# Optimization experiments

Measured on AMD Instinct MI355X. Metric: run time of the kernel, lower is better.

The kernel has to match this reference:

```python
import jax, jax.numpy as jnp
import numpy as np

N_NODES = 100000
N_EDGES = 300000
D_IN = 256
D_OUT = 256
NEG_SLOPE = 0.2


def setup_inputs() -> dict:
    key = jax.random.key(0)
    ks = jax.random.split(key, 6)
    feat = jax.random.normal(ks[0], (N_NODES, D_IN), dtype=jnp.float32)
    # xavier-normal-ish init scale
    scale = (2.0 / (D_IN + D_OUT)) ** 0.5
    W_src = jax.random.normal(ks[1], (D_IN, D_OUT), dtype=jnp.float32) * scale
    b_src = jnp.zeros((D_OUT,), dtype=jnp.float32)
    W_dst = jax.random.normal(ks[2], (D_IN, D_OUT), dtype=jnp.float32) * scale
    b_dst = jnp.zeros((D_OUT,), dtype=jnp.float32)
    attn = jax.random.normal(ks[3], (D_OUT,), dtype=jnp.float32) * scale
    src = jax.random.randint(ks[4], (N_EDGES,), 0, N_NODES, dtype=jnp.int32)
    dst = jax.random.randint(ks[5], (N_EDGES,), 0, N_NODES, dtype=jnp.int32)
    return {"feat": feat, "W_src": W_src, "b_src": b_src,
            "W_dst": W_dst, "b_dst": b_dst, "attn": attn,
            "src": src, "dst": dst}


def reference(feat, W_src, b_src, W_dst, b_dst, attn, src, dst):
    N = feat.shape[0]
    # node projections (dense GEMMs)
    el = feat @ W_src + b_src          # [N, D_OUT]  (feat_src / 'el')
    er = feat @ W_dst + b_dst          # [N, D_OUT]  (feat_dst / 'er')
    # edge-wise u_add_v + LeakyReLU, then attention dot
    e = jax.nn.leaky_relu(el[src] + er[dst], NEG_SLOPE)  # [E, D_OUT]
    score = e @ attn                    # [E]  ((e*attn).sum(-1))
    # edge softmax segmented by destination node
    smax = jax.ops.segment_max(score, dst, num_segments=N)   # [N]
    ex = jnp.exp(score - smax[dst])                           # [E]
    ssum = jax.ops.segment_sum(ex, dst, num_segments=N)      # [N]
    a = ex / ssum[dst]                                        # [E]
    # weighted scatter-sum aggregation: u_mul_e('el','a') -> sum per dst
    out = jax.ops.segment_sum(el[src] * a[:, None], dst, num_segments=N)
    return out  # [N, D_OUT]
```

## Files before the change

kernel.cpp:

```cpp
#include <hip/hip_runtime.h>
#include <cstdint>
#include <cmath>

#define D 256
#define NEG 0.2f
#define BK 64
#define NT (D/BK)

typedef __attribute__((ext_vector_type(8))) __bf16 bf16x8;
typedef __attribute__((ext_vector_type(8))) unsigned short ushort8;
typedef __attribute__((ext_vector_type(4))) float f32x4;

__device__ __forceinline__ unsigned short f2bf(float f){
    unsigned u = __float_as_uint(f);
    return (unsigned short)((u + 0x7fffu + ((u >> 16) & 1u)) >> 16);
}
__device__ __forceinline__ float b2f(unsigned short u){
    return __uint_as_float(((unsigned)u) << 16);
}

__device__ __forceinline__ void gload_lds16(const void* g, void* l){
    __builtin_amdgcn_global_load_lds(
        (const __attribute__((address_space(1))) unsigned int*)g,
        (__attribute__((address_space(3))) unsigned int*)l, 16, 0, 0);
}

__global__ __launch_bounds__(256) void prep_w_kernel(
    const float* __restrict__ Wsrc, const float* __restrict__ Wdst,
    const float* __restrict__ bsrc, const float* __restrict__ bdst,
    unsigned short* __restrict__ WT, float* __restrict__ biascat)
{
    int idx = blockIdx.x*256 + threadIdx.x;
    int col = idx >> 5;
    int u   = idx & 31;
    int gu  = (u & 24) | ((u ^ col) & 7);
    const float* W = (col < 256) ? Wsrc : Wdst;
    int c = col & 255;
    ushort8 o;
    #pragma unroll
    for (int j = 0; j < 8; ++j)
        o[j] = f2bf(W[(size_t)(gu*8 + j)*D + c]);
    *(ushort8*)(WT + (size_t)col*D + u*8) = o;
    if (idx < 512) biascat[idx] = (idx < 256) ? bsrc[idx] : bdst[idx-256];
}

__global__ __launch_bounds__(256) void prep_feat_kernel(
    const float* __restrict__ feat, unsigned short* __restrict__ featb, int N, int NPAD)
{
    int total = NPAD * 32;
    for (int idx = blockIdx.x*256 + threadIdx.x; idx < total; idx += gridDim.x*256){
        int r = idx >> 5;
        int u = idx & 31;
        ushort8 o;
        if (r < N){
            int gu = (u & 24) | ((u ^ r) & 7);
            const float* s = feat + (size_t)r*D + gu*8;
            float4 a = *(const float4*)s;
            float4 b = *(const float4*)(s + 4);
            o[0]=f2bf(a.x); o[1]=f2bf(a.y); o[2]=f2bf(a.z); o[3]=f2bf(a.w);
            o[4]=f2bf(b.x); o[5]=f2bf(b.y); o[6]=f2bf(b.z); o[7]=f2bf(b.w);
        } else {
            #pragma unroll
            for (int j = 0; j < 8; ++j) o[j] = 0;
        }
        *(ushort8*)(featb + (size_t)r*D + u*8) = o;
    }
}

__global__ __launch_bounds__(256) void proj_mfma_kernel(
    const unsigned short* __restrict__ featb, const unsigned short* __restrict__ WT,
    const float* __restrict__ biascat,
    unsigned short* __restrict__ el16, unsigned short* __restrict__ er16, int N)
{
    __shared__ unsigned short As[2][128*BK];
    __shared__ unsigned short Bs[2][128*BK];

    const int b    = blockIdx.x;
    const int xcd  = b & 7;
    const int s    = b >> 3;
    const int p    = (s >> 2)*8 + xcd;
    const int c    = s & 3;
    const int row0 = p * 128;
    const int col0 = c * 128;

    const int tid  = threadIdx.x;
    const int wave = tid >> 6;
    const int lane = tid & 63;
    const int wr = (wave >> 1) * 64;
    const int wc = (wave & 1) * 64;
    const int l15 = lane & 15;
    const int kg  = lane >> 4;

    const int sr = (wave << 3) + (lane >> 3);
    const int sc = (lane & 7) * 8;

    f32x4 acc[4][4] = {};

    #pragma unroll
    for (int r4 = 0; r4 < 4; ++r4) {
        int ar = r4*32 + sr;
        gload_lds16(featb + (size_t)(row0 + ar)*D + 0 + sc, &As[0][(r4*32 + wave*8)*BK]);
        gload_lds16(WT    + (size_t)(col0 + ar)*D + 0 + sc, &Bs[0][(r4*32 + wave*8)*BK]);
    }

    for (int t = 0; t < NT; ++t) {
        const int cur = t & 1;
        if (t + 1 < NT) {
            int k0 = (t + 1) * BK;
            #pragma unroll
            for (int r4 = 0; r4 < 4; ++r4) {
                int ar = r4*32 + sr;
                gload_lds16(featb + (size_t)(row0 + ar)*D + k0 + sc,
                            &As[cur ^ 1][(r4*32 + wave*8)*BK]);
                gload_lds16(WT    + (size_t)(col0 + ar)*D + k0 + sc,
                            &Bs[cur ^ 1][(r4*32 + wave*8)*BK]);
            }
            asm volatile("s_waitcnt vmcnt(8)" ::: "memory");
        } else {
            asm volatile("s_waitcnt vmcnt(0)" ::: "memory");
        }
        __builtin_amdgcn_s_barrier();
        __builtin_amdgcn_sched_barrier(0);

        #pragma unroll
        for (int ks = 0; ks < 2; ++ks) {
            bf16x8 af[4], bfr[4];
            #pragma unroll
            for (int m = 0; m < 4; ++m){
                int row = wr + m*16 + l15;
                int cc = ((kg + ks*4) ^ (row & 7)) * 8;
                af[m] = *(const bf16x8*)&As[cur][row*BK + cc];
            }
            #pragma unroll
            for (int n = 0; n < 4; ++n){
                int row = wc + n*16 + l15;
                int cc = ((kg + ks*4) ^ (row & 7)) * 8;
                bfr[n] = *(const bf16x8*)&Bs[cur][row*BK + cc];
            }
            #pragma unroll
            for (int m = 0; m < 4; ++m)
                #pragma unroll
                for (int n = 0; n < 4; ++n)
                    acc[m][n] = __builtin_amdgcn_mfma_f32_16x16x32_bf16(bfr[n], af[m], acc[m][n], 0, 0, 0);
        }
        __builtin_amdgcn_sched_barrier(0);
        __builtin_amdgcn_s_barrier();
    }

    unsigned short* __restrict__ dstp = (col0 < 256) ? el16 : er16;
    const int ccbase = col0 & 255;
    #pragma unroll
    for (int m = 0; m < 4; ++m) {
        int row = row0 + wr + m*16 + l15;
        if (row >= N) continue;
        #pragma unroll
        for (int n = 0; n < 4; ++n) {
            int cw = wc + n*16 + kg*4;
            float4 b4 = *(const float4*)(biascat + col0 + cw);
            ushort4 o;
            o.x = f2bf(acc[m][n][0] + b4.x);
            o.y = f2bf(acc[m][n][1] + b4.y);
            o.z = f2bf(acc[m][n][2] + b4.z);
            o.w = f2bf(acc[m][n][3] + b4.w);
            *(ushort4*)(dstp + (size_t)row*D + ccbase + cw) = o;
        }
    }
}

__global__ void count_kernel(const int* __restrict__ dst, int* __restrict__ deg, int E){
    int e = blockIdx.x*blockDim.x + threadIdx.x;
    if (e < E) atomicAdd(&deg[dst[e]], 1);
}

__global__ __launch_bounds__(256) void scan1_kernel(const int* __restrict__ deg,
                                                    int* __restrict__ incl,
                                                    int* __restrict__ bsum, int N){
    __shared__ int s[256];
    int i = blockIdx.x*256 + threadIdx.x;
    int v = (i < N) ? deg[i] : 0;
    s[threadIdx.x] = v;
    __syncthreads();
    #pragma unroll
    for (int off = 1; off < 256; off <<= 1){
        int t = (threadIdx.x >= off) ? s[threadIdx.x - off] : 0;
        __syncthreads();
        s[threadIdx.x] += t;
        __syncthreads();
    }
    if (i < N) incl[i] = s[threadIdx.x];
    if (threadIdx.x == 255) bsum[blockIdx.x] = s[255];
}

__global__ __launch_bounds__(512) void scan2_kernel(int* __restrict__ bsum, int nb){
    __shared__ int s[512];
    int t = threadIdx.x;
    int v = (t < nb) ? bsum[t] : 0;
    s[t] = v;
    __syncthreads();
    #pragma unroll
    for (int off = 1; off < 512; off <<= 1){
        int u = (t >= off) ? s[t - off] : 0;
        __syncthreads();
        s[t] += u;
        __syncthreads();
    }
    if (t < nb) bsum[t] = s[t] - v;
}

__global__ __launch_bounds__(256) void scan3_kernel(const int* __restrict__ deg,
                                                    const int* __restrict__ incl,
                                                    const int* __restrict__ bsum,
                                                    int* __restrict__ rowstart,
                                                    int* __restrict__ cursor, int N){
    int i = blockIdx.x*256 + threadIdx.x;
    if (i < N){
        int st = incl[i] - deg[i] + bsum[blockIdx.x];
        rowstart[i] = st;
        cursor[i]   = st;
    }
}

__global__ void scatter_kernel(const int* __restrict__ dst, const int* __restrict__ src,
                               int* __restrict__ cursor, int* __restrict__ srcs, int E){
    int e = blockIdx.x*blockDim.x + threadIdx.x;
    if (e < E){
        int pos = atomicAdd(&cursor[dst[e]], 1);
        srcs[pos] = src[e];
    }
}

__global__ __launch_bounds__(256) void gat_node_kernel(
    const unsigned short* __restrict__ el16, const unsigned short* __restrict__ er16,
    const float* __restrict__ attn, const int* __restrict__ srcs,
    const int* __restrict__ rowstart, const int* __restrict__ degv,
    float* __restrict__ out, int N)
{
    int node = blockIdx.x*4 + (threadIdx.x >> 6);
    if (node >= N) return;
    int lane = threadIdx.x & 63;
    float4 o = make_float4(0.f,0.f,0.f,0.f);
    int deg = degv[node];
    float* op = out + (size_t)node*D + lane*4;
    if (deg == 0){ *(float4*)op = o; return; }

    ushort4 rv = *(const ushort4*)(er16 + (size_t)node*D + lane*4);
    float4 r4 = make_float4(b2f(rv.x), b2f(rv.y), b2f(rv.z), b2f(rv.w));
    float4 a4 = *(const float4*)(attn + lane*4);
    int start = rowstart[node];

    float m = -INFINITY, ssum = 0.f;
    for (int base = 0; base < deg; base += 4){
        int cnt = deg - base; if (cnt > 4) cnt = 4;
        float4 l[4]; float p[4];
        #pragma unroll
        for (int j = 0; j < 4; ++j){
            int k = base + j; if (k >= deg) k = deg - 1;
            int sn = srcs[start + k];
            ushort4 lv = *(const ushort4*)(el16 + (size_t)sn*D + lane*4);
            l[j] = make_float4(b2f(lv.x), b2f(lv.y), b2f(lv.z), b2f(lv.w));
        }
        #pragma unroll
        for (int j = 0; j < 4; ++j){
            float x, pp = 0.f;
            x = l[j].x + r4.x; pp += (x > 0.f ? x : NEG*x) * a4.x;
            x = l[j].y + r4.y; pp += (x > 0.f ? x : NEG*x) * a4.y;
            x = l[j].z + r4.z; pp += (x > 0.f ? x : NEG*x) * a4.z;
            x = l[j].w + r4.w; pp += (x > 0.f ? x : NEG*x) * a4.w;
            p[j] = pp;
        }
        #pragma unroll
        for (int off = 32; off > 0; off >>= 1){
            #pragma unroll
            for (int j = 0; j < 4; ++j) p[j] += __shfl_xor(p[j], off, 64);
        }
        #pragma unroll
        for (int j = 0; j < 4; ++j){
            if (j >= cnt) break;
            float newm  = fmaxf(m, p[j]);
            float scale = __expf(m - newm);
            float w     = __expf(p[j] - newm);
            ssum = ssum*scale + w;
            o.x = o.x*scale + w*l[j].x;
            o.y = o.y*scale + w*l[j].y;
            o.z = o.z*scale + w*l[j].z;
            o.w = o.w*scale + w*l[j].w;
            m = newm;
        }
    }
    float inv = 1.f/ssum;
    o.x *= inv; o.y *= inv; o.z *= inv; o.w *= inv;
    *(float4*)op = o;
}

extern "C" void kernel_launch(void* const* d_in, const int* in_sizes, int n_in,
                              void* d_out, int out_size, void* d_ws, size_t ws_size,
                              hipStream_t stream)
{
    const float* feat = (const float*)d_in[0];
    const float* Wsrc = (const float*)d_in[1];
    const float* bsrc = (const float*)d_in[2];
    const float* Wdst = (const float*)d_in[3];
    const float* bdst = (const float*)d_in[4];
    const float* attn = (const float*)d_in[5];
    const int*   src  = (const int*)d_in[6];
    const int*   dst  = (const int*)d_in[7];
    const int N = in_sizes[0] / D;
    const int E = in_sizes[6];
    const int NPAD = ((N + 1023)/1024)*1024;
    const int NP = NPAD / 128;
    float* out = (float*)d_out;

    unsigned short* el16 = (unsigned short*)d_ws;
    unsigned short* er16 = el16 + (size_t)N*D;
    int* deg      = (int*)(er16 + (size_t)N*D);
    int* incl     = deg + N;
    int* rowstart = incl + N;
    int* cursor   = rowstart + N;
    int* bsum     = cursor + N;
    int* srcs     = bsum + 512;
    unsigned short* WT = (unsigned short*)(srcs + E);
    float* biascat = (float*)(WT + (size_t)512*D);
    unsigned short* featb = (unsigned short*)(biascat + 512);

    const int nb = (N + 255)/256;

    hipMemsetAsync(deg, 0, (size_t)N*sizeof(int), stream);

    prep_w_kernel<<<64, 256, 0, stream>>>(Wsrc, Wdst, bsrc, bdst, WT, biascat);
    prep_feat_kernel<<<4096, 256, 0, stream>>>(feat, featb, N, NPAD);

    proj_mfma_kernel<<<4*NP, 256, 0, stream>>>(featb, WT, biascat, el16, er16, N);

    count_kernel<<<(E + 255)/256, 256, 0, stream>>>(dst, deg, E);
    scan1_kernel<<<nb, 256, 0, stream>>>(deg, incl, bsum, N);
    scan2_kernel<<<1, 512, 0, stream>>>(bsum, nb);
    scan3_kernel<<<nb, 256, 0, stream>>>(deg, incl, bsum, rowstart, cursor, N);
    scatter_kernel<<<(E + 255)/256, 256, 0, stream>>>(dst, src, cursor, srcs, E);

    gat_node_kernel<<<(N + 3)/4, 256, 0, stream>>>(el16, er16, attn, srcs,
                                                   rowstart, deg, out, N);
}
```

Measured before the change: 186.9 us.

## Replace LDS double-buffered GEMM staging with direct global fragment loads

The projection GEMM no longer stages feat and weight tiles through shared memory with async global-to-LDS copies, double buffering and barriers. Each wave now loads its MFMA fragments straight from global memory, and the XOR swizzle in the prep kernels is dropped so the data is stored in plain row-major bf16 order. This removes LDS traffic, barriers and waitcnt stalls. In exchange it loses data reuse across waves within a block, adds redundant global/L2 reads, and leaves the loads without an explicit prefetch pipeline.

```diff
diff --git a/kernel.cpp b/kernel.cpp
--- a/kernel.cpp
+++ b/kernel.cpp
@@ -4,8 +4,6 @@
 
 #define D 256
 #define NEG 0.2f
-#define BK 64
-#define NT (D/BK)
 
 typedef __attribute__((ext_vector_type(8))) __bf16 bf16x8;
 typedef __attribute__((ext_vector_type(8))) unsigned short ushort8;
@@ -17,12 +15,6 @@
 }
 __device__ __forceinline__ float b2f(unsigned short u){
     return __uint_as_float(((unsigned)u) << 16);
-}
-
-__device__ __forceinline__ void gload_lds16(const void* g, void* l){
-    __builtin_amdgcn_global_load_lds(
-        (const __attribute__((address_space(1))) unsigned int*)g,
-        (__attribute__((address_space(3))) unsigned int*)l, 16, 0, 0);
 }
 
 __global__ __launch_bounds__(256) void prep_w_kernel(
@@ -33,13 +25,12 @@
     int idx = blockIdx.x*256 + threadIdx.x;
     int col = idx >> 5;
     int u   = idx & 31;
-    int gu  = (u & 24) | ((u ^ col) & 7);
     const float* W = (col < 256) ? Wsrc : Wdst;
     int c = col & 255;
     ushort8 o;
     #pragma unroll
     for (int j = 0; j < 8; ++j)
-        o[j] = f2bf(W[(size_t)(gu*8 + j)*D + c]);
+        o[j] = f2bf(W[(size_t)(u*8 + j)*D + c]);
     *(ushort8*)(WT + (size_t)col*D + u*8) = o;
     if (idx < 512) biascat[idx] = (idx < 256) ? bsrc[idx] : bdst[idx-256];
 }
@@ -53,8 +44,7 @@
         int u = idx & 31;
         ushort8 o;
         if (r < N){
-            int gu = (u & 24) | ((u ^ r) & 7);
-            const float* s = feat + (size_t)r*D + gu*8;
+            const float* s = feat + (size_t)r*D + u*8;
             float4 a = *(const float4*)s;
             float4 b = *(const float4*)(s + 4);
             o[0]=f2bf(a.x); o[1]=f2bf(a.y); o[2]=f2bf(a.z); o[3]=f2bf(a.w);
@@ -72,9 +62,6 @@
     const float* __restrict__ biascat,
     unsigned short* __restrict__ el16, unsigned short* __restrict__ er16, int N)
 {
-    __shared__ unsigned short As[2][128*BK];
-    __shared__ unsigned short Bs[2][128*BK];
-
     const int b    = blockIdx.x;
     const int xcd  = b & 7;
     const int s    = b >> 3;
@@ -91,60 +78,31 @@
     const int l15 = lane & 15;
     const int kg  = lane >> 4;
 
-    const int sr = (wave << 3) + (lane >> 3);
-    const int sc = (lane & 7) * 8;
+    const unsigned short* __restrict__ ar[4];
+    const unsigned short* __restrict__ br[4];
+    #pragma unroll
+    for (int m = 0; m < 4; ++m) ar[m] = featb + (size_t)(row0 + wr + m*16 + l15)*D;
+    #pragma unroll
+    for (int n = 0; n < 4; ++n) br[n] = WT    + (size_t)(col0 + wc + n*16 + l15)*D;
 
     f32x4 acc[4][4] = {};
 
     #pragma unroll
-    for (int r4 = 0; r4 < 4; ++r4) {
-        int ar = r4*32 + sr;
-        gload_lds16(featb + (size_t)(row0 + ar)*D + 0 + sc, &As[0][(r4*32 + wave*8)*BK]);
-        gload_lds16(WT    + (size_t)(col0 + ar)*D + 0 + sc, &Bs[0][(r4*32 + wave*8)*BK]);
-    }
-
-    for (int t = 0; t < NT; ++t) {
-        const int cur = t & 1;
-        if (t + 1 < NT) {
-            int k0 = (t + 1) * BK;
-            #pragma unroll
-            for (int r4 = 0; r4 < 4; ++r4) {
-                int ar = r4*32 + sr;
-                gload_lds16(featb + (size_t)(row0 + ar)*D + k0 + sc,
-                            &As[cur ^ 1][(r4*32 + wave*8)*BK]);
-                gload_lds16(WT    + (size_t)(col0 + ar)*D + k0 + sc,
-                            &Bs[cur ^ 1][(r4*32 + wave*8)*BK]);
-            }
-            asm volatile("s_waitcnt vmcnt(8)" ::: "memory");
-        } else {
-            asm volatile("s_waitcnt vmcnt(0)" ::: "memory");
-        }
-        __builtin_amdgcn_s_barrier();
-        __builtin_amdgcn_sched_barrier(0);
-
+    for (int t = 0; t < 4; ++t) {
         #pragma unroll
         for (int ks = 0; ks < 2; ++ks) {
-            bf16x8 af[4], bfr[4];
-            #pragma unroll
-            for (int m = 0; m < 4; ++m){
-                int row = wr + m*16 + l15;
-                int cc = ((kg + ks*4) ^ (row & 7)) * 8;
-                af[m] = *(const bf16x8*)&As[cur][row*BK + cc];
-            }
-            #pragma unroll
-            for (int n = 0; n < 4; ++n){
-                int row = wc + n*16 + l15;
-                int cc = ((kg + ks*4) ^ (row & 7)) * 8;
-                bfr[n] = *(const bf16x8*)&Bs[cur][row*BK + cc];
-            }
+            const int ko = t*64 + (kg + ks*4)*8;
+            bf16x8 af[4], bf[4];
+            #pragma unroll
+            for (int m = 0; m < 4; ++m) af[m] = *(const bf16x8*)(ar[m] + ko);
+            #pragma unroll
+            for (int n = 0; n < 4; ++n) bf[n] = *(const bf16x8*)(br[n] + ko);
             #pragma unroll
             for (int m = 0; m < 4; ++m)
                 #pragma unroll
                 for (int n = 0; n < 4; ++n)
-                    acc[m][n] = __builtin_amdgcn_mfma_f32_16x16x32_bf16(bfr[n], af[m], acc[m][n], 0, 0, 0);
-        }
-        __builtin_amdgcn_sched_barrier(0);
-        __builtin_amdgcn_s_barrier();
+                    acc[m][n] = __builtin_amdgcn_mfma_f32_16x16x32_bf16(bf[n], af[m], acc[m][n], 0, 0, 0);
+        }
     }
 
     unsigned short* __restrict__ dstp = (col0 < 256) ? el16 : er16;
```

Result: slower. 250.0 us (+33.7%).
